# Kernel optimization log

Hardware: AMD Instinct MI355X
Metric: run time of the kernel (lower is better)

The kernel has to match this reference:

```python
import jax, jax.numpy as jnp
import numpy as np

def setup_inputs() -> dict:
    key = jax.random.key(0)
    k1, k2 = jax.random.split(key)
    B, H, Q = 65536, 1024, 8
    hidden_state = jax.random.normal(k1, (B, H), dtype=jnp.float32)
    # nn.Linear(hidden_dim, n_qubits): weight [Q, H], bias [Q]
    W = jax.random.normal(k2, (Q, H), dtype=jnp.float32) * (1.0 / np.sqrt(H))
    b = jnp.zeros((Q,), dtype=jnp.float32)
    return {"hidden_state": hidden_state, "W": W, "b": b}

def reference(hidden_state, W, b):
    # Linear projection: [B, H] @ [H, Q] + [Q] -> [B, Q] (RX rotation angles)
    theta = jnp.einsum('bh,qh->bq', hidden_state, W) + b
    # RX(theta) on |0> gives P(|0>) = cos^2(theta/2) per qubit.
    # probs(all wires)[0] = P(|00..0>) = prod_i cos^2(theta_i/2)  (closed form,
    # equivalent to the full 2^n state-vector simulation in the original).
    c = jnp.cos(theta * 0.5)
    p0 = jnp.prod(c * c, axis=-1)  # [B]
    return jnp.mean(1.0 - p0)
```

## Files before the change

### kernel.cpp

```cpp
#include <hip/hip_runtime.h>


#define HDIM 1024
#define QN 8
#define RPB 64
#define SEGS 4
#define SEG_H 256
#define CHUNK 32
#define ROUNDS 8
#define ROW_STRIDE 36

__global__ __launch_bounds__(256, 4)
void qreg_kernel(const float* __restrict__ hidden,
                 const float* __restrict__ W,
                 const float* __restrict__ bias,
                 float* __restrict__ out) {
    __shared__ __align__(16) float tile[SEGS * RPB * ROW_STRIDE];

    const int tid  = threadIdx.x;
    const int lane = tid & 63;
    const int seg  = __builtin_amdgcn_readfirstlane(tid >> 6);
    const int row_base = blockIdx.x * RPB;

    const int s_row = (tid >> 3) & 7;
    const int s_col = tid & 7;

    const float* gbase = hidden + (size_t)row_base * HDIM + seg * SEG_H + s_col * 4;

    float4 stage[8];
#pragma unroll
    for (int i = 0; i < 8; ++i) {
        stage[i] = *reinterpret_cast<const float4*>(gbase + (size_t)(s_row + 8 * i) * HDIM);
    }

    float acc[QN];
#pragma unroll
    for (int q = 0; q < QN; ++q) acc[q] = 0.f;

#pragma unroll
    for (int k = 0; k < ROUNDS; ++k) {
#pragma unroll
        for (int i = 0; i < 8; ++i) {
            int r = s_row + 8 * i;
            *reinterpret_cast<float4*>(&tile[(seg * RPB + r) * ROW_STRIDE + s_col * 4]) = stage[i];
        }
        __syncthreads();

        if (k < ROUNDS - 1) {
#pragma unroll
            for (int i = 0; i < 8; ++i) {
                stage[i] = *reinterpret_cast<const float4*>(
                    gbase + (size_t)(s_row + 8 * i) * HDIM + (k + 1) * CHUNK);
            }
        }

        const float* xrow = &tile[(seg * RPB + lane) * ROW_STRIDE];
        const int hbase = seg * SEG_H + k * CHUNK;
#pragma unroll
        for (int j = 0; j < CHUNK / 4; ++j) {
            float4 x = *reinterpret_cast<const float4*>(&xrow[j * 4]);
#pragma unroll
            for (int q = 0; q < QN; ++q) {
                const float* wq = W + q * HDIM + hbase + j * 4;
                acc[q] += x.x * wq[0] + x.y * wq[1] + x.z * wq[2] + x.w * wq[3];
            }
        }
        __syncthreads();
    }

    float* red = tile;
#pragma unroll
    for (int q = 0; q < QN; ++q)
        red[(seg * RPB + lane) * QN + q] = acc[q];
    __syncthreads();

    if (seg == 0) {
        float p0 = 1.f;
#pragma unroll
        for (int q = 0; q < QN; ++q) {
            float th = red[(0 * RPB + lane) * QN + q]
                     + red[(1 * RPB + lane) * QN + q]
                     + red[(2 * RPB + lane) * QN + q]
                     + red[(3 * RPB + lane) * QN + q]
                     + bias[q];
            float c = __cosf(0.5f * th);
            p0 *= c * c;
        }
        float contrib = 1.f - p0;
#pragma unroll
        for (int off = 32; off > 0; off >>= 1)
            contrib += __shfl_down(contrib, off);
        if (lane == 0)
            atomicAdd(out, contrib * (1.0f / 65536.0f));
    }
}

extern "C" void kernel_launch(void* const* d_in, const int* in_sizes, int n_in,
                              void* d_out, int out_size, void* d_ws, size_t ws_size,
                              hipStream_t stream) {
    const float* hidden = (const float*)d_in[0];
    const float* W      = (const float*)d_in[1];
    const float* bias   = (const float*)d_in[2];
    float* out          = (float*)d_out;

    hipMemsetAsync(out, 0, sizeof(float), stream);
    qreg_kernel<<<65536 / RPB, 256, 0, stream>>>(hidden, W, bias, out);
}
```

Baseline: 433.3 us.

## Load hidden tiles directly into LDS with 1024-thread blocks and split columns across waves

The register-staged prefetch is replaced by direct global-to-LDS loads (global_load_lds, 16 bytes per lane), staging a 64x256 tile per round in four rounds. Blocks grow to 16 waves, and each wave multiplies a 16-column slice of every row against W. Partial sums then go through a two-level LDS reduction before the cosine product and the atomic. This is meant to cut VGPR staging and raise memory-level parallelism, but it drops the overlap of the next tile's load with compute and uses about 66KB of LDS per block, which limits blocks per CU.

```diff
diff --git a/kernel.cpp b/kernel.cpp
--- a/kernel.cpp
+++ b/kernel.cpp
@@ -4,34 +4,21 @@
 #define HDIM 1024
 #define QN 8
 #define RPB 64
-#define SEGS 4
-#define SEG_H 256
-#define CHUNK 32
-#define ROUNDS 8
-#define ROW_STRIDE 36
+#define CHUNK 256
+#define ROUNDS 4
+#define ROW_STRIDE 260
 
-__global__ __launch_bounds__(256, 4)
+__global__ __launch_bounds__(1024, 8)
 void qreg_kernel(const float* __restrict__ hidden,
                  const float* __restrict__ W,
                  const float* __restrict__ bias,
                  float* __restrict__ out) {
-    __shared__ __align__(16) float tile[SEGS * RPB * ROW_STRIDE];
+    __shared__ __align__(16) float tile[RPB * ROW_STRIDE];
 
     const int tid  = threadIdx.x;
     const int lane = tid & 63;
-    const int seg  = __builtin_amdgcn_readfirstlane(tid >> 6);
-    const int row_base = blockIdx.x * RPB;
-
-    const int s_row = (tid >> 3) & 7;
-    const int s_col = tid & 7;
-
-    const float* gbase = hidden + (size_t)row_base * HDIM + seg * SEG_H + s_col * 4;
-
-    float4 stage[8];
-#pragma unroll
-    for (int i = 0; i < 8; ++i) {
-        stage[i] = *reinterpret_cast<const float4*>(gbase + (size_t)(s_row + 8 * i) * HDIM);
-    }
+    const int w    = __builtin_amdgcn_readfirstlane(tid >> 6);
+    const size_t row_base = (size_t)blockIdx.x * RPB;
 
     float acc[QN];
 #pragma unroll
@@ -40,57 +27,62 @@
 #pragma unroll
     for (int k = 0; k < ROUNDS; ++k) {
 #pragma unroll
-        for (int i = 0; i < 8; ++i) {
-            int r = s_row + 8 * i;
-            *reinterpret_cast<float4*>(&tile[(seg * RPB + r) * ROW_STRIDE + s_col * 4]) = stage[i];
+        for (int i = 0; i < 4; ++i) {
+            const int r = 4 * w + i;
+            const float* g = hidden + (row_base + r) * HDIM + k * CHUNK + lane * 4;
+            __builtin_amdgcn_global_load_lds(
+                (const __attribute__((address_space(1))) void*)g,
+                (__attribute__((address_space(3))) void*)&tile[r * ROW_STRIDE],
+                16, 0, 0);
         }
         __syncthreads();
 
-        if (k < ROUNDS - 1) {
+        float4 x0 = *reinterpret_cast<const float4*>(&tile[lane * ROW_STRIDE + w * 16 + 0]);
+        float4 x1 = *reinterpret_cast<const float4*>(&tile[lane * ROW_STRIDE + w * 16 + 4]);
+        float4 x2 = *reinterpret_cast<const float4*>(&tile[lane * ROW_STRIDE + w * 16 + 8]);
+        float4 x3 = *reinterpret_cast<const float4*>(&tile[lane * ROW_STRIDE + w * 16 + 12]);
+
+        const float* wbase = W + k * CHUNK + w * 16;
 #pragma unroll
-            for (int i = 0; i < 8; ++i) {
-                stage[i] = *reinterpret_cast<const float4*>(
-                    gbase + (size_t)(s_row + 8 * i) * HDIM + (k + 1) * CHUNK);
-            }
-        }
-
-        const float* xrow = &tile[(seg * RPB + lane) * ROW_STRIDE];
-        const int hbase = seg * SEG_H + k * CHUNK;
-#pragma unroll
-        for (int j = 0; j < CHUNK / 4; ++j) {
-            float4 x = *reinterpret_cast<const float4*>(&xrow[j * 4]);
-#pragma unroll
-            for (int q = 0; q < QN; ++q) {
-                const float* wq = W + q * HDIM + hbase + j * 4;
-                acc[q] += x.x * wq[0] + x.y * wq[1] + x.z * wq[2] + x.w * wq[3];
-            }
+        for (int q = 0; q < QN; ++q) {
+            const float* wq = wbase + q * HDIM;
+            acc[q] += x0.x * wq[0]  + x0.y * wq[1]  + x0.z * wq[2]  + x0.w * wq[3]
+                    + x1.x * wq[4]  + x1.y * wq[5]  + x1.z * wq[6]  + x1.w * wq[7]
+                    + x2.x * wq[8]  + x2.y * wq[9]  + x2.z * wq[10] + x2.w * wq[11]
+                    + x3.x * wq[12] + x3.y * wq[13] + x3.z * wq[14] + x3.w * wq[15];
         }
         __syncthreads();
     }
 
-    float* red = tile;
+    float* part = tile;
 #pragma unroll
     for (int q = 0; q < QN; ++q)
-        red[(seg * RPB + lane) * QN + q] = acc[q];
+        part[(w * RPB + lane) * 9 + q] = acc[q];
     __syncthreads();
 
-    if (seg == 0) {
+    float* theta = tile + 9216;
+    if (tid < 512) {
+        const int r = tid >> 3, q = tid & 7;
+        float th = bias[q];
+#pragma unroll
+        for (int ww = 0; ww < 16; ++ww)
+            th += part[(ww * RPB + r) * 9 + q];
+        theta[r * 8 + q] = th;
+    }
+    __syncthreads();
+
+    if (tid < 64) {
         float p0 = 1.f;
 #pragma unroll
         for (int q = 0; q < QN; ++q) {
-            float th = red[(0 * RPB + lane) * QN + q]
-                     + red[(1 * RPB + lane) * QN + q]
-                     + red[(2 * RPB + lane) * QN + q]
-                     + red[(3 * RPB + lane) * QN + q]
-                     + bias[q];
-            float c = __cosf(0.5f * th);
+            float c = __cosf(0.5f * theta[tid * 8 + q]);
             p0 *= c * c;
         }
         float contrib = 1.f - p0;
 #pragma unroll
         for (int off = 32; off > 0; off >>= 1)
             contrib += __shfl_down(contrib, off);
-        if (lane == 0)
+        if (tid == 0)
             atomicAdd(out, contrib * (1.0f / 65536.0f));
     }
 }
@@ -104,5 +96,5 @@
     float* out          = (float*)d_out;
 
     hipMemsetAsync(out, 0, sizeof(float), stream);
-    qreg_kernel<<<65536 / RPB, 256, 0, stream>>>(hidden, W, bias, out);
+    qreg_kernel<<<65536 / RPB, 1024, 0, stream>>>(hidden, W, bias, out);
 }
```

Result: faster. 364.1 us (-16.0%).
